# Optimization experiments

Hardware: AMD Instinct MI355X
Metric: run time of the kernel (lower is better)

## Reference

```python
import jax, jax.numpy as jnp
import numpy as np

H, OC = 64, 32  # hidden_channels, out_channels
N0, N1, N2, N3 = 65536, 16384, 4096, 1024
K3, K2 = 27, 8  # kernel taps: 3^3 stride-1 conv, 2^3 stride-2 conv


def _spconv(feat, nmap, W, b):
    # gather-GEMM sparse conv: feat [N_in,C], nmap [N_out,K] indices, W [K,C,D]
    g = feat[nmap]                       # [N_out, K, C]
    return jnp.einsum('nkc,kcd->nd', g, W) + b


def setup_inputs() -> dict:
    key = jax.random.key(0)
    ks = jax.random.split(key, 16)
    f32 = jnp.float32
    d = {
        'x': jax.random.normal(ks[0], (N0, H), f32),
        'Wg0': jax.random.normal(ks[1], (OC, H), f32) / np.sqrt(OC),
        'bg0': jnp.zeros((H,), f32),
        'Wg1': jax.random.normal(ks[2], (OC, H), f32) / np.sqrt(OC),
        'bg1': jnp.zeros((H,), f32),
        'Wout': jax.random.normal(ks[3], (H, OC), f32) / np.sqrt(H),
        'bout': jnp.zeros((OC,), f32),
        'WA': jax.random.normal(ks[4], (K3, H, H), f32) / np.sqrt(K3 * H),
        'bA': jnp.zeros((H,), f32),
        'WB': jax.random.normal(ks[5], (K3, H, H), f32) / np.sqrt(K3 * H),
        'bB': jnp.zeros((H,), f32),
        'WD': jax.random.normal(ks[6], (K2, H, H), f32) / np.sqrt(K2 * H),
        'bD': jnp.zeros((H,), f32),
        'WC': jax.random.normal(ks[7], (K3, H, H), f32) / np.sqrt(K3 * H),
        'bC': jnp.zeros((H,), f32),
        'nmap0': jax.random.randint(ks[8], (N0, K3), 0, N0, jnp.int32),
        'nmap1': jax.random.randint(ks[9], (N1, K3), 0, N1, jnp.int32),
        'nmap2': jax.random.randint(ks[10], (N2, K3), 0, N2, jnp.int32),
        'nmap3': jax.random.randint(ks[11], (N3, K3), 0, N3, jnp.int32),
        'nd0': jax.random.randint(ks[12], (N1, K2), 0, N0, jnp.int32),
        'nd1': jax.random.randint(ks[13], (N2, K2), 0, N1, jnp.int32),
        'nd2': jax.random.randint(ks[14], (N3, K2), 0, N2, jnp.int32),
    }
    return d


def reference(x, Wg0, bg0, Wg1, bg1, Wout, bout, WA, bA, WB, bB, WD, bD, WC, bC,
              nmap0, nmap1, nmap2, nmap3, nd0, nd1, nd2):
    nmaps = [nmap0, nmap1, nmap2, nmap3]
    nds = [nd0, nd1, nd2]
    outs = []
    cx = x
    hx = cx @ Wout + bout            # block_out (hidden -> out_channels)
    outs.append(hx)
    for s in range(3):               # unrolled recurrent while-loop (3 scales)
        # sub-step 0: gate + two stride-1 sparse convs at same coords
        g = jax.nn.sigmoid(hx @ Wg0 + bg0)
        cx = g * cx
        cx = jax.nn.relu(_spconv(cx, nmaps[s], WA, bA))
        cx = jax.nn.relu(_spconv(cx, nmaps[s], WB, bB))
        hx = cx @ Wout + bout
        outs.append(hx)
        # sub-step 1: gate + stride-2 downsample conv + stride-1 conv
        g = jax.nn.sigmoid(hx @ Wg1 + bg1)
        cx = g * cx
        cx = jax.nn.relu(_spconv(cx, nds[s], WD, bD))      # N_s -> N_{s+1}
        cx = jax.nn.relu(_spconv(cx, nmaps[s + 1], WC, bC))
        hx = cx @ Wout + bout
        outs.append(hx)
    return tuple(outs)
```

## Files before the change

### kernel.cpp

```cpp
#include <hip/hip_runtime.h>
#include <hip/hip_bf16.h>

typedef __attribute__((ext_vector_type(8))) short short8;
typedef __attribute__((ext_vector_type(4))) float f32x4;

#define N0 65536
#define N1 16384
#define N2 4096
#define N3 1024

__device__ __forceinline__ float bfu(unsigned short u) {
    unsigned int x = ((unsigned int)u) << 16;
    return __builtin_bit_cast(float, x);
}
__device__ __forceinline__ unsigned short fbf(float f) {
    return __builtin_bit_cast(unsigned short, __float2bfloat16(f));
}

__global__ void prep_all(const float* __restrict__ A, const float* __restrict__ B,
                         const float* __restrict__ C, const float* __restrict__ D,
                         const float* __restrict__ Wg0, const float* __restrict__ Wg1,
                         const float* __restrict__ bB, const float* __restrict__ bC,
                         const float* __restrict__ bout, const float* __restrict__ bg0,
                         const float* __restrict__ bg1,
                         __hip_bfloat16* __restrict__ Wt,
                         __hip_bfloat16* __restrict__ Wgb,
                         float* __restrict__ pack)
{
    int i = blockIdx.x * 256 + threadIdx.x;
    if (i < 89 * 4096) {
        int k = i >> 12, r = i & 4095, d = r >> 6, c = r & 63;
        const float* src; int kl;
        if (k < 27)      { src = A; kl = k; }
        else if (k < 54) { src = B; kl = k - 27; }
        else if (k < 81) { src = C; kl = k - 54; }
        else             { src = D; kl = k - 81; }
        Wt[i] = __float2bfloat16(src[(kl << 12) + (c << 6) + d]);
        return;
    }
    int j = i - 89 * 4096;
    if (j < 2048) { Wgb[j] = __float2bfloat16(Wg1[j]); return; }
    j -= 2048;
    if (j < 2048) { Wgb[2048 + j] = __float2bfloat16(Wg0[j]); return; }
    j -= 2048;
    if (j < 160) {
        pack[j] = (j < 64) ? bB[j] : (j < 96) ? bout[j - 64] : bg1[j - 96];
        return;
    }
    j -= 160;
    if (j < 160) {
        pack[160 + j] = (j < 64) ? bC[j] : (j < 96) ? bout[j - 64] : bg0[j - 96];
    }
}

__global__ __launch_bounds__(256) void spconv_mfma(
    const __hip_bfloat16* __restrict__ feat, const int* __restrict__ nmap,
    const __hip_bfloat16* __restrict__ Wt, __hip_bfloat16* __restrict__ outp,
    const float* __restrict__ bias, int Nout, int K, int mode,
    const float* __restrict__ Woutg, const __hip_bfloat16* __restrict__ Wgb,
    const float* __restrict__ pack, float* __restrict__ hx_out,
    __hip_bfloat16* __restrict__ gout)
{
    __shared__ int ldsm[10240];
    short* AbufS = (short*)ldsm;
    short* BbufS = (short*)(ldsm + 4096);
    int*   jl    = ldsm + 8192;
    short* WgL   = (short*)(ldsm + 8192);
    float* packL = (float*)(ldsm + 8192 + 1024);

    const int t = threadIdx.x;
    const int w = t >> 6, l = t & 63;
    const int lr = l & 15, lh = l >> 4;
    const int row0 = blockIdx.x * 64;

    for (int i = t; i < K * 64; i += 256) {
        int k = i >> 6, r = i & 63;
        jl[i] = nmap[(size_t)(row0 + r) * K + k];
    }
    __syncthreads();

    const int rr0 = (w << 4) + (l >> 3);
    const int qq = (l & 7) ^ (l >> 3);

    auto stage = [&](int buf, int k) {
        const __hip_bfloat16* Wk = Wt + (size_t)k * 4096;
#pragma unroll
        for (int i = 0; i < 2; ++i) {
            int rr = rr0 + (i << 3);
            int j = jl[(k << 6) + rr];
            __builtin_amdgcn_global_load_lds(
                (const __attribute__((address_space(1))) void*)(feat + ((size_t)j << 6) + (qq << 3)),
                (__attribute__((address_space(3))) void*)(AbufS + buf * 4096 + (w << 10) + (i << 9)),
                16, 0, 0);
            __builtin_amdgcn_global_load_lds(
                (const __attribute__((address_space(1))) void*)(Wk + (rr << 6) + (qq << 3)),
                (__attribute__((address_space(3))) void*)(BbufS + buf * 4096 + (w << 10) + (i << 9)),
                16, 0, 0);
        }
    };

    auto stage_epi = [&](int buf) {
        short* dstW = BbufS + buf * 4096;
#pragma unroll
        for (int i = 0; i < 2; ++i) {
            int s = t + i * 256;
            int r = s >> 3, qp = s & 7;
            int q = qp ^ (r >> 4);
            __builtin_amdgcn_global_load_lds(
                (const __attribute__((address_space(1))) void*)(Woutg + (r << 5) + (q << 2)),
                (__attribute__((address_space(3))) void*)(dstW + (w << 9) + (i << 11)),
                16, 0, 0);
        }
        __builtin_amdgcn_global_load_lds(
            (const __attribute__((address_space(1))) void*)(Wgb + (t << 3)),
            (__attribute__((address_space(3))) void*)(WgL + (w << 9)),
            16, 0, 0);
        if (t < 40)
            __builtin_amdgcn_global_load_lds(
                (const __attribute__((address_space(1))) void*)(pack + (t << 2)),
                (__attribute__((address_space(3))) void*)packL,
                16, 0, 0);
    };

    f32x4 acc[4] = {};
    const int arow = (w << 4) + lr;

#define COMPUTE(cur_)                                                            \
    {                                                                            \
        const short* Ab = AbufS + (cur_) * 4096;                                 \
        const short* Bb = BbufS + (cur_) * 4096;                                 \
        _Pragma("unroll")                                                        \
        for (int kk = 0; kk < 2; ++kk) {                                         \
            int q = (kk << 2) + lh;                                              \
            short8 a = *(const short8*)&Ab[(arow << 6) + ((q ^ (arow & 7)) << 3)];\
            _Pragma("unroll")                                                    \
            for (int ct = 0; ct < 4; ++ct) {                                     \
                int dr = (ct << 4) + lr;                                         \
                short8 b = *(const short8*)&Bb[(dr << 6) + ((q ^ (dr & 7)) << 3)];\
                acc[ct] = __builtin_amdgcn_mfma_f32_16x16x32_bf16(a, b, acc[ct], 0, 0, 0); \
            }                                                                    \
        }                                                                        \
    }

    stage(0, 0);

    int cur = 0;
    for (int k = 0; k < K; ++k) {
        if (k + 1 < K) {
            stage(cur ^ 1, k + 1);
            asm volatile("s_waitcnt vmcnt(4)" ::: "memory");
        } else {
            if (mode == 3) stage_epi(cur ^ 1);
            asm volatile("s_waitcnt vmcnt(0)" ::: "memory");
        }
        asm volatile("s_barrier" ::: "memory");
        COMPUTE(cur);
        asm volatile("s_barrier" ::: "memory");
        cur ^= 1;
    }
#undef COMPUTE

    if (mode != 3) {
#pragma unroll
        for (int ct = 0; ct < 4; ++ct) {
            int col = (ct << 4) + lr;
            float bv = (mode == 2) ? bias[col] : 0.f;
#pragma unroll
            for (int rr = 0; rr < 4; ++rr) {
                int row = row0 + (w << 4) + (lh << 2) + rr;
                float v = acc[ct][rr];
                if (mode == 2) v = fmaxf(v + bv, 0.f);
                outp[((size_t)row << 6) + col] = __float2bfloat16(v);
            }
        }
        return;
    }

    short* tl = AbufS;
    float* WoutL = (float*)(BbufS + cur * 4096);

#pragma unroll
    for (int ct = 0; ct < 4; ++ct) {
        int col = (ct << 4) + lr;
        float bv = packL[col];
#pragma unroll
        for (int rr = 0; rr < 4; ++rr) {
            int rl = (w << 4) + (lh << 2) + rr;
            float v = fmaxf(acc[ct][rr] + bv, 0.f);
            tl[rl * 72 + col] = (short)fbf(v);
        }
    }
    __syncthreads();

    const int g4 = t & 3, rloc = t >> 2;
    const short* trow = tl + rloc * 72 + (g4 << 4);
    float tv[16];
    {
        short8 u0 = *(const short8*)trow;
        short8 u1 = *(const short8*)(trow + 8);
#pragma unroll
        for (int j = 0; j < 8; ++j) {
            tv[j]     = bfu((unsigned short)u0[j]);
            tv[8 + j] = bfu((unsigned short)u1[j]);
        }
    }
    float ph[32];
#pragma unroll
    for (int d = 0; d < 32; ++d) ph[d] = 0.f;
#pragma unroll
    for (int i = 0; i < 16; ++i) {
        float tc = tv[i];
        const float* wrow = WoutL + (((g4 << 4) + i) << 5);
#pragma unroll
        for (int q = 0; q < 8; ++q) {
            f32x4 wv = *(const f32x4*)&wrow[(q ^ g4) << 2];
            ph[q * 4 + 0] = fmaf(tc, wv[0], ph[q * 4 + 0]);
            ph[q * 4 + 1] = fmaf(tc, wv[1], ph[q * 4 + 1]);
            ph[q * 4 + 2] = fmaf(tc, wv[2], ph[q * 4 + 2]);
            ph[q * 4 + 3] = fmaf(tc, wv[3], ph[q * 4 + 3]);
        }
    }
#pragma unroll
    for (int m = 1; m < 4; m <<= 1) {
#pragma unroll
        for (int d = 0; d < 32; ++d) ph[d] += __shfl_xor(ph[d], m);
    }
#pragma unroll
    for (int d = 0; d < 32; ++d) ph[d] += packL[64 + d];

    {
        float* ho = hx_out + ((size_t)(row0 + rloc) << 5);
#pragma unroll
        for (int G = 0; G < 4; ++G)
            if (g4 == G) {
                float4 v0 = {ph[G * 8 + 0], ph[G * 8 + 1], ph[G * 8 + 2], ph[G * 8 + 3]};
                float4 v1 = {ph[G * 8 + 4], ph[G * 8 + 5], ph[G * 8 + 6], ph[G * 8 + 7]};
                ((float4*)ho)[G * 2 + 0] = v0;
                ((float4*)ho)[G * 2 + 1] = v1;
            }
    }

    float ga[16];
#pragma unroll
    for (int j = 0; j < 16; ++j) ga[j] = packL[96 + (g4 << 4) + j];
#pragma unroll
    for (int d = 0; d < 32; ++d) {
        float hd = ph[d];
        const short* wg = WgL + (d << 6) + (g4 << 4);
        short8 w0 = *(const short8*)wg;
        short8 w1 = *(const short8*)(wg + 8);
#pragma unroll
        for (int j = 0; j < 8; ++j) {
            ga[j]     = fmaf(hd, bfu((unsigned short)w0[j]), ga[j]);
            ga[8 + j] = fmaf(hd, bfu((unsigned short)w1[j]), ga[8 + j]);
        }
    }
    {
        short8 o0, o1;
#pragma unroll
        for (int j = 0; j < 8; ++j) {
            float g0 = 1.f / (1.f + __expf(-ga[j]));
            float g1 = 1.f / (1.f + __expf(-ga[8 + j]));
            o0[j] = (short)fbf(g0 * tv[j]);
            o1[j] = (short)fbf(g1 * tv[8 + j]);
        }
        short* go = (short*)gout + ((size_t)(row0 + rloc) << 6) + (g4 << 4);
        *(short8*)go = o0;
        *(short8*)(go + 8) = o1;
    }
}

__global__ __launch_bounds__(256) void epi_full(
    const void* __restrict__ srcp, int smode, int ch, const float* __restrict__ bconv,
    const float* __restrict__ Wout, const float* __restrict__ bout,
    const float* __restrict__ Wg, const float* __restrict__ bg,
    float* __restrict__ hx_out, __hip_bfloat16* __restrict__ gout, int N)
{
    __shared__ float Woutl[64 * 32];
    __shared__ float Wgl[32 * 64];
    __shared__ float boutl[32];
    __shared__ float bgl[64];
    __shared__ float bcl[64];

    const int t = threadIdx.x;
    for (int i = t; i < 2048; i += 256) {
        int r = i >> 5, col = i & 31;
        int q = col >> 2, e = col & 3;
        Woutl[(r << 5) + ((q ^ (r >> 3)) << 2) + e] = Wout[i];
        Wgl[i] = Wg[i];
    }
    if (t < 32) boutl[t] = bout[t];
    if (t >= 64 && t < 128) bgl[t - 64] = bg[t - 64];
    if (t >= 128 && t < 192) bcl[t - 128] = bconv ? bconv[t - 128] : 0.f;
    __syncthreads();

    const int g = t & 7;
    const int row = blockIdx.x * 32 + (t >> 3);
    const int c0 = g << 3;

    float tv[8];
    if (smode == 0) {
        const ushort4* sb = (const ushort4*)((const __hip_bfloat16*)srcp + ((size_t)row << 6) + c0);
        ushort4 v0 = sb[0], v1 = sb[1];
        tv[0] = bfu(v0.x); tv[1] = bfu(v0.y); tv[2] = bfu(v0.z); tv[3] = bfu(v0.w);
        tv[4] = bfu(v1.x); tv[5] = bfu(v1.y); tv[6] = bfu(v1.z); tv[7] = bfu(v1.w);
    } else {
        const float4* sf = (const float4*)((const float*)srcp + ((size_t)row << 6) + c0);
        float4 a = sf[0], b = sf[1];
        tv[0] = a.x; tv[1] = a.y; tv[2] = a.z; tv[3] = a.w;
        tv[4] = b.x; tv[5] = b.y; tv[6] = b.z; tv[7] = b.w;
    }
    if (smode != 2) {
#pragma unroll
        for (int i = 0; i < 8; ++i) tv[i] = fmaxf(tv[i] + bcl[c0 + i], 0.f);
    }

    float ph[32];
#pragma unroll
    for (int d = 0; d < 32; ++d) ph[d] = 0.f;
#pragma unroll
    for (int i = 0; i < 8; ++i) {
        float tc = tv[i];
        const float* wr = &Woutl[(c0 + i) << 5];
#pragma unroll
        for (int q = 0; q < 8; ++q) {
            f32x4 wv = *(const f32x4*)&wr[(q ^ g) << 2];
            ph[q * 4 + 0] = fmaf(tc, wv[0], ph[q * 4 + 0]);
            ph[q * 4 + 1] = fmaf(tc, wv[1], ph[q * 4 + 1]);
            ph[q * 4 + 2] = fmaf(tc, wv[2], ph[q * 4 + 2]);
            ph[q * 4 + 3] = fmaf(tc, wv[3], ph[q * 4 + 3]);
        }
    }
#pragma unroll
    for (int m = 1; m < 8; m <<= 1) {
#pragma unroll
        for (int d = 0; d < 32; ++d) ph[d] += __shfl_xor(ph[d], m);
    }
#pragma unroll
    for (int d = 0; d < 32; ++d) ph[d] += boutl[d];

    {
        float* ho = hx_out + ((size_t)row << 5);
#pragma unroll
        for (int G = 0; G < 8; ++G)
            if (g == G) {
                float4 v = {ph[G * 4 + 0], ph[G * 4 + 1], ph[G * 4 + 2], ph[G * 4 + 3]};
                ((float4*)ho)[G] = v;
            }
    }

    float ga[8];
#pragma unroll
    for (int j = 0; j < 8; ++j) ga[j] = bgl[c0 + j];
#pragma unroll
    for (int d = 0; d < 32; ++d) {
        float hd = ph[d];
        const float* wr = &Wgl[(d << 6) + c0];
        f32x4 w0 = *(const f32x4*)&wr[0];
        f32x4 w1 = *(const f32x4*)&wr[4];
        ga[0] = fmaf(hd, w0[0], ga[0]); ga[1] = fmaf(hd, w0[1], ga[1]);
        ga[2] = fmaf(hd, w0[2], ga[2]); ga[3] = fmaf(hd, w0[3], ga[3]);
        ga[4] = fmaf(hd, w1[0], ga[4]); ga[5] = fmaf(hd, w1[1], ga[5]);
        ga[6] = fmaf(hd, w1[2], ga[6]); ga[7] = fmaf(hd, w1[3], ga[7]);
    }
    {
        unsigned short ob[8];
#pragma unroll
        for (int j = 0; j < 8; ++j) {
            float gg = 1.f / (1.f + __expf(-ga[j]));
            ob[j] = fbf(gg * tv[j]);
        }
        ushort4* go = (ushort4*)(gout + ((size_t)row << 6) + c0);
        ushort4 o0 = {ob[0], ob[1], ob[2], ob[3]};
        ushort4 o1 = {ob[4], ob[5], ob[6], ob[7]};
        go[0] = o0; go[1] = o1;
    }
}

extern "C" void kernel_launch(void* const* d_in, const int* in_sizes, int n_in,
                              void* d_out, int out_size, void* d_ws, size_t ws_size,
                              hipStream_t stream)
{
    const float* x    = (const float*)d_in[0];
    const float* Wg0  = (const float*)d_in[1];
    const float* bg0  = (const float*)d_in[2];
    const float* Wg1  = (const float*)d_in[3];
    const float* bg1  = (const float*)d_in[4];
    const float* Wout = (const float*)d_in[5];
    const float* bout = (const float*)d_in[6];
    const float* WA   = (const float*)d_in[7];
    const float* bA   = (const float*)d_in[8];
    const float* WB   = (const float*)d_in[9];
    const float* bB   = (const float*)d_in[10];
    const float* WD   = (const float*)d_in[11];
    const float* bD   = (const float*)d_in[12];
    const float* WC   = (const float*)d_in[13];
    const float* bC   = (const float*)d_in[14];
    const int* nmap[4] = {(const int*)d_in[15], (const int*)d_in[16],
                          (const int*)d_in[17], (const int*)d_in[18]};
    const int* ndm[3]  = {(const int*)d_in[19], (const int*)d_in[20],
                          (const int*)d_in[21]};

    float* out = (float*)d_out;
    __hip_bfloat16* featbf0 = (__hip_bfloat16*)d_ws;
    __hip_bfloat16* featbf1 = featbf0 + (size_t)N0 * 64;
    __hip_bfloat16* WAt = featbf1 + (size_t)N0 * 64;
    __hip_bfloat16* WBt = WAt + 27 * 4096;
    __hip_bfloat16* WCt = WBt + 27 * 4096;
    __hip_bfloat16* WDt = WCt + 27 * 4096;
    __hip_bfloat16* Wgb = WDt + 8 * 4096;
    float* packw = (float*)(Wgb + 4096);

    const int Ns[4] = {N0, N1, N2, N3};
    size_t off[7];
    off[0] = 0;
    off[1] = off[0] + (size_t)N0 * 32;
    off[2] = off[1] + (size_t)N0 * 32;
    off[3] = off[2] + (size_t)N1 * 32;
    off[4] = off[3] + (size_t)N1 * 32;
    off[5] = off[4] + (size_t)N2 * 32;
    off[6] = off[5] + (size_t)N2 * 32;

    hipLaunchKernelGGL(prep_all, dim3((89 * 4096 + 4416 + 255) / 256), dim3(256), 0, stream,
                       WA, WB, WC, WD, Wg0, Wg1, bB, bC, bout, bg0, bg1,
                       WAt, Wgb, packw);

    auto conv2 = [&](const __hip_bfloat16* fin, const int* nm,
                     const __hip_bfloat16* Wt, int Nout, int K,
                     const float* bias2, __hip_bfloat16* dst) {
        hipLaunchKernelGGL(spconv_mfma, dim3(Nout / 64), dim3(256), 0, stream,
                           fin, nm, Wt, dst, bias2, Nout, K, 2,
                           (const float*)nullptr, (const __hip_bfloat16*)nullptr,
                           (const float*)nullptr, (float*)nullptr,
                           (__hip_bfloat16*)nullptr);
    };
    auto conv3 = [&](const __hip_bfloat16* fin, const int* nm,
                     const __hip_bfloat16* Wt, int Nout, int K,
                     const float* packp, const __hip_bfloat16* Wgbp,
                     float* hx, __hip_bfloat16* gdst) {
        hipLaunchKernelGGL(spconv_mfma, dim3(Nout / 64), dim3(256), 0, stream,
                           fin, nm, Wt, (__hip_bfloat16*)nullptr,
                           (const float*)nullptr, Nout, K, 3,
                           Wout, Wgbp, packp, hx, gdst);
    };

    hipLaunchKernelGGL(epi_full, dim3(N0 / 32), dim3(256), 0, stream,
                       (const void*)x, 2, 1, (const float*)nullptr, Wout, bout, Wg0, bg0,
                       out + off[0], featbf0, N0);

    for (int s = 0; s < 3; ++s) {
        int N = Ns[s], Nn = Ns[s + 1];

        conv2(featbf0, nmap[s], WAt, N, 27, bA, featbf1);
        conv3(featbf1, nmap[s], WBt, N, 27, packw, Wgb, out + off[s * 2 + 1], featbf0);

        conv2(featbf0, ndm[s], WDt, Nn, 8, bD, featbf1);
        conv3(featbf1, nmap[s + 1], WCt, Nn, 27, packw + 160, Wgb + 2048,
              out + off[s * 2 + 2], featbf0);
    }
}
```

Before: 300.2 us.

## Split-K small sparse convs across grid and unfuse largest-scale epilogue

Splits the small-scale sparse convolutions across kernel taps using a second grid dimension. The partial sums go to an fp32 workspace and a new reduce kernel adds bias and ReLU. This gives more blocks on the small levels, which would otherwise leave most CUs idle. At the largest scale, the B conv now writes bf16 and runs a separate epilogue kernel instead of the fused mode-3 path, and the fused path moves to its own kernel. The cost is extra launches and extra global traffic for the partial sums.

```diff
diff --git a/kernel.cpp b/kernel.cpp
--- a/kernel.cpp
+++ b/kernel.cpp
@@ -55,8 +55,115 @@
 
 __global__ __launch_bounds__(256) void spconv_mfma(
     const __hip_bfloat16* __restrict__ feat, const int* __restrict__ nmap,
-    const __hip_bfloat16* __restrict__ Wt, __hip_bfloat16* __restrict__ outp,
-    const float* __restrict__ bias, int Nout, int K, int mode,
+    const __hip_bfloat16* __restrict__ Wt, void* __restrict__ outp,
+    const float* __restrict__ bias, int Nout, int K, int mode)
+{
+    __shared__ short Abuf[2][64 * 64];
+    __shared__ short Bbuf[2][64 * 64];
+    __shared__ int jl[27 * 64];
+
+    const int t = threadIdx.x;
+    const int w = t >> 6, l = t & 63;
+    const int lr = l & 15, lh = l >> 4;
+    const int row0 = blockIdx.x * 64;
+    const int per = (K + gridDim.y - 1) / gridDim.y;
+    const int kb0 = blockIdx.y * per;
+    const int nk = min(K, kb0 + per) - kb0;
+
+    for (int i = t; i < nk * 64; i += 256) {
+        int k = i >> 6, r = i & 63;
+        jl[i] = nmap[(size_t)(row0 + r) * K + (kb0 + k)];
+    }
+    __syncthreads();
+
+    const int rr0 = (w << 4) + (l >> 3);
+    const int qq = (l & 7) ^ (l >> 3);
+
+    auto stage = [&](int buf, int k) {
+        const __hip_bfloat16* Wk = Wt + (size_t)(kb0 + k) * 4096;
+#pragma unroll
+        for (int i = 0; i < 2; ++i) {
+            int rr = rr0 + (i << 3);
+            int j = jl[(k << 6) + rr];
+            __builtin_amdgcn_global_load_lds(
+                (const __attribute__((address_space(1))) void*)(feat + ((size_t)j << 6) + (qq << 3)),
+                (__attribute__((address_space(3))) void*)&Abuf[buf][(w << 10) + (i << 9)],
+                16, 0, 0);
+            __builtin_amdgcn_global_load_lds(
+                (const __attribute__((address_space(1))) void*)(Wk + (rr << 6) + (qq << 3)),
+                (__attribute__((address_space(3))) void*)&Bbuf[buf][(w << 10) + (i << 9)],
+                16, 0, 0);
+        }
+    };
+
+    f32x4 acc[4] = {};
+    const int arow = (w << 4) + lr;
+
+#define COMPUTE(cur_)                                                            \
+    {                                                                            \
+        const short* Ab = Abuf[cur_];                                            \
+        const short* Bb = Bbuf[cur_];                                            \
+        _Pragma("unroll")                                                        \
+        for (int kk = 0; kk < 2; ++kk) {                                         \
+            int q = (kk << 2) + lh;                                              \
+            short8 a = *(const short8*)&Ab[(arow << 6) + ((q ^ (arow & 7)) << 3)];\
+            _Pragma("unroll")                                                    \
+            for (int ct = 0; ct < 4; ++ct) {                                     \
+                int dr = (ct << 4) + lr;                                         \
+                short8 b = *(const short8*)&Bb[(dr << 6) + ((q ^ (dr & 7)) << 3)];\
+                acc[ct] = __builtin_amdgcn_mfma_f32_16x16x32_bf16(a, b, acc[ct], 0, 0, 0); \
+            }                                                                    \
+        }                                                                        \
+    }
+
+    stage(0, 0);
+
+    int cur = 0;
+    for (int k = 0; k < nk; ++k) {
+        if (k + 1 < nk) {
+            stage(cur ^ 1, k + 1);
+            asm volatile("s_waitcnt vmcnt(4)" ::: "memory");
+        } else {
+            asm volatile("s_waitcnt vmcnt(0)" ::: "memory");
+        }
+        asm volatile("s_barrier" ::: "memory");
+        COMPUTE(cur)
+        asm volatile("s_barrier" ::: "memory");
+        cur ^= 1;
+    }
+#undef COMPUTE
+
+    if (mode == 1) {
+        float* o32 = (float*)outp + (size_t)blockIdx.y * ((size_t)Nout << 6);
+#pragma unroll
+        for (int ct = 0; ct < 4; ++ct) {
+            int col = (ct << 4) + lr;
+#pragma unroll
+            for (int rr = 0; rr < 4; ++rr) {
+                int row = row0 + (w << 4) + (lh << 2) + rr;
+                o32[((size_t)row << 6) + col] = acc[ct][rr];
+            }
+        }
+    } else {
+        __hip_bfloat16* ob = (__hip_bfloat16*)outp;
+#pragma unroll
+        for (int ct = 0; ct < 4; ++ct) {
+            int col = (ct << 4) + lr;
+            float bv = (mode == 2) ? bias[col] : 0.f;
+#pragma unroll
+            for (int rr = 0; rr < 4; ++rr) {
+                int row = row0 + (w << 4) + (lh << 2) + rr;
+                float v = acc[ct][rr];
+                if (mode == 2) v = fmaxf(v + bv, 0.f);
+                ob[((size_t)row << 6) + col] = __float2bfloat16(v);
+            }
+        }
+    }
+}
+
+__global__ __launch_bounds__(256) void spconv_fused(
+    const __hip_bfloat16* __restrict__ feat, const int* __restrict__ nmap,
+    const __hip_bfloat16* __restrict__ Wt, int K,
     const float* __restrict__ Woutg, const __hip_bfloat16* __restrict__ Wgb,
     const float* __restrict__ pack, float* __restrict__ hx_out,
     __hip_bfloat16* __restrict__ gout)
@@ -150,31 +257,15 @@
             stage(cur ^ 1, k + 1);
             asm volatile("s_waitcnt vmcnt(4)" ::: "memory");
         } else {
-            if (mode == 3) stage_epi(cur ^ 1);
+            stage_epi(cur ^ 1);
             asm volatile("s_waitcnt vmcnt(0)" ::: "memory");
         }
         asm volatile("s_barrier" ::: "memory");
-        COMPUTE(cur);
+        COMPUTE(cur)
         asm volatile("s_barrier" ::: "memory");
         cur ^= 1;
     }
 #undef COMPUTE
-
-    if (mode != 3) {
-#pragma unroll
-        for (int ct = 0; ct < 4; ++ct) {
-            int col = (ct << 4) + lr;
-            float bv = (mode == 2) ? bias[col] : 0.f;
-#pragma unroll
-            for (int rr = 0; rr < 4; ++rr) {
-                int row = row0 + (w << 4) + (lh << 2) + rr;
-                float v = acc[ct][rr];
-                if (mode == 2) v = fmaxf(v + bv, 0.f);
-                outp[((size_t)row << 6) + col] = __float2bfloat16(v);
-            }
-        }
-        return;
-    }
 
     short* tl = AbufS;
     float* WoutL = (float*)(BbufS + cur * 4096);
@@ -268,6 +359,26 @@
         *(short8*)go = o0;
         *(short8*)(go + 8) = o1;
     }
+}
+
+__global__ void reduce_relu_bf(const float* __restrict__ in, const float* __restrict__ bias,
+                               __hip_bfloat16* __restrict__ outb, int nv, int ch)
+{
+    int i = blockIdx.x * blockDim.x + threadIdx.x;
+    if (i >= nv) return;
+    const float4* in4 = (const float4*)in;
+    float4 s = in4[i];
+    for (int c = 1; c < ch; ++c) {
+        float4 v = in4[(size_t)c * nv + i];
+        s.x += v.x; s.y += v.y; s.z += v.z; s.w += v.w;
+    }
+    int cb = (i << 2) & 63;
+    ushort4 o;
+    o.x = fbf(fmaxf(s.x + bias[cb + 0], 0.f));
+    o.y = fbf(fmaxf(s.y + bias[cb + 1], 0.f));
+    o.z = fbf(fmaxf(s.z + bias[cb + 2], 0.f));
+    o.w = fbf(fmaxf(s.w + bias[cb + 3], 0.f));
+    ((ushort4*)outb)[i] = o;
 }
 
 __global__ __launch_bounds__(256) void epi_full(
@@ -307,6 +418,14 @@
     } else {
         const float4* sf = (const float4*)((const float*)srcp + ((size_t)row << 6) + c0);
         float4 a = sf[0], b = sf[1];
+        if (smode == 3) {
+            const size_t cs = (size_t)N * 16;
+            for (int c = 1; c < ch; ++c) {
+                float4 u = sf[c * cs], v = sf[c * cs + 1];
+                a.x += u.x; a.y += u.y; a.z += u.z; a.w += u.w;
+                b.x += v.x; b.y += v.y; b.z += v.z; b.w += v.w;
+            }
+        }
         tv[0] = a.x; tv[1] = a.y; tv[2] = a.z; tv[3] = a.w;
         tv[4] = b.x; tv[5] = b.y; tv[6] = b.z; tv[7] = b.w;
     }
@@ -404,7 +523,9 @@
     float* out = (float*)d_out;
     __hip_bfloat16* featbf0 = (__hip_bfloat16*)d_ws;
     __hip_bfloat16* featbf1 = featbf0 + (size_t)N0 * 64;
-    __hip_bfloat16* WAt = featbf1 + (size_t)N0 * 64;
+    __hip_bfloat16* convbf  = featbf1 + (size_t)N0 * 64;
+    float* conv32 = (float*)(convbf + (size_t)N0 * 64);
+    __hip_bfloat16* WAt = (__hip_bfloat16*)(conv32 + (size_t)N2 * 64 * 8);
     __hip_bfloat16* WBt = WAt + 27 * 4096;
     __hip_bfloat16* WCt = WBt + 27 * 4096;
     __hip_bfloat16* WDt = WCt + 27 * 4096;
@@ -425,23 +546,24 @@
                        WA, WB, WC, WD, Wg0, Wg1, bB, bC, bout, bg0, bg1,
                        WAt, Wgb, packw);
 
-    auto conv2 = [&](const __hip_bfloat16* fin, const int* nm,
-                     const __hip_bfloat16* Wt, int Nout, int K,
-                     const float* bias2, __hip_bfloat16* dst) {
-        hipLaunchKernelGGL(spconv_mfma, dim3(Nout / 64), dim3(256), 0, stream,
-                           fin, nm, Wt, dst, bias2, Nout, K, 2,
-                           (const float*)nullptr, (const __hip_bfloat16*)nullptr,
-                           (const float*)nullptr, (float*)nullptr,
-                           (__hip_bfloat16*)nullptr);
+    auto chunks = [&](int Nout, int K) -> int {
+        if (Nout >= 16384) return 1;
+        if (Nout == 4096) return (K == 27) ? 4 : 2;
+        return (K == 27) ? 7 : 4;
     };
-    auto conv3 = [&](const __hip_bfloat16* fin, const int* nm,
-                     const __hip_bfloat16* Wt, int Nout, int K,
-                     const float* packp, const __hip_bfloat16* Wgbp,
-                     float* hx, __hip_bfloat16* gdst) {
-        hipLaunchKernelGGL(spconv_mfma, dim3(Nout / 64), dim3(256), 0, stream,
-                           fin, nm, Wt, (__hip_bfloat16*)nullptr,
-                           (const float*)nullptr, Nout, K, 3,
-                           Wout, Wgbp, packp, hx, gdst);
+    auto convAD = [&](const __hip_bfloat16* fin, const int* nm,
+                      const __hip_bfloat16* Wt, int Nout, int K,
+                      const float* bias2, __hip_bfloat16* dst) -> int {
+        int ch = chunks(Nout, K);
+        if (ch > 1) {
+            hipLaunchKernelGGL(spconv_mfma, dim3(Nout / 64, ch), dim3(256), 0, stream,
+                               fin, nm, Wt, (void*)conv32, (const float*)nullptr,
+                               Nout, K, 1);
+            return ch;
+        }
+        hipLaunchKernelGGL(spconv_mfma, dim3(Nout / 64, 1), dim3(256), 0, stream,
+                           fin, nm, Wt, (void*)dst, bias2, Nout, K, 2);
+        return 0;
     };
 
     hipLaunchKernelGGL(epi_full, dim3(N0 / 32), dim3(256), 0, stream,
@@ -451,11 +573,31 @@
     for (int s = 0; s < 3; ++s) {
         int N = Ns[s], Nn = Ns[s + 1];
 
-        conv2(featbf0, nmap[s], WAt, N, 27, bA, featbf1);
-        conv3(featbf1, nmap[s], WBt, N, 27, packw, Wgb, out + off[s * 2 + 1], featbf0);
-
-        conv2(featbf0, ndm[s], WDt, Nn, 8, bD, featbf1);
-        conv3(featbf1, nmap[s + 1], WCt, Nn, 27, packw + 160, Wgb + 2048,
-              out + off[s * 2 + 2], featbf0);
-    }
-}
+        int mA = convAD(featbf0, nmap[s], WAt, N, 27, bA, featbf1);
+        if (mA)
+            hipLaunchKernelGGL(reduce_relu_bf, dim3((N * 16 + 255) / 256), dim3(256), 0, stream,
+                               conv32, bA, featbf1, N * 16, mA);
+
+        if (N >= 65536) {
+            hipLaunchKernelGGL(spconv_mfma, dim3(N / 64, 1), dim3(256), 0, stream,
+                               featbf1, nmap[s], WBt, (void*)convbf,
+                               (const float*)nullptr, N, 27, 0);
+            hipLaunchKernelGGL(epi_full, dim3(N / 32), dim3(256), 0, stream,
+                               (const void*)convbf, 0, 1, bB, Wout, bout, Wg1, bg1,
+                               out + off[s * 2 + 1], featbf0, N);
+        } else {
+            hipLaunchKernelGGL(spconv_fused, dim3(N / 64), dim3(256), 0, stream,
+                               featbf1, nmap[s], WBt, 27,
+                               Wout, Wgb, packw, out + off[s * 2 + 1], featbf0);
+        }
+
+        int mD = convAD(featbf0, ndm[s], WDt, Nn, 8, bD, featbf1);
+        if (mD)
+            hipLaunchKernelGGL(reduce_relu_bf, dim3((Nn * 16 + 255) / 256), dim3(256), 0, stream,
+                               conv32, bD, featbf1, Nn * 16, mD);
+
+        hipLaunchKernelGGL(spconv_fused, dim3(Nn / 64), dim3(256), 0, stream,
+                           featbf1, nmap[s + 1], WCt, 27,
+                           Wout, Wgb + 2048, packw + 160, out + off[s * 2 + 2], featbf0);
+    }
+}
```

Result: faster. 265.1 us (-11.7%).
